# Optimization experiments

Hardware: AMD Instinct MI355X
Metric: run time of the kernel (lower is better)

The kernel has to match this reference:

```python
import jax, jax.numpy as jnp
import numpy as np

N_NODES, N_EDGES, NUM_GRAPHS = 50000, 800000, 64
F_DIM, H_DIM, N_LAYERS, N_CLASSES = 64, 64, 3, 16
EPS = 1e-5  # StdAggregation epsilon (PyG)


def setup_inputs() -> dict:
    key = jax.random.key(0)
    ks = jax.random.split(key, 12)
    s = 0.05
    x = jax.random.normal(ks[0], (N_NODES, F_DIM), jnp.float32)
    edge_index = jax.random.randint(ks[1], (2, N_EDGES), 0, N_NODES, dtype=jnp.int32)
    batch = jnp.sort(jax.random.randint(ks[2], (N_NODES,), 0, NUM_GRAPHS, dtype=jnp.int32))
    # per-layer PNAConv params (towers=1): pre Linear(2F->F), post Linear(13F->H), lin Linear(H->H)
    pre_w = jax.random.normal(ks[3], (N_LAYERS, F_DIM, 2 * F_DIM), jnp.float32) * s
    pre_b = jnp.zeros((N_LAYERS, F_DIM), jnp.float32)
    post_w = jax.random.normal(ks[4], (N_LAYERS, H_DIM, 13 * F_DIM), jnp.float32) * s
    post_b = jnp.zeros((N_LAYERS, H_DIM), jnp.float32)
    lin_w = jax.random.normal(ks[5], (N_LAYERS, H_DIM, H_DIM), jnp.float32) * s
    lin_b = jnp.zeros((N_LAYERS, H_DIM), jnp.float32)
    mlp_w1 = jax.random.normal(ks[6], (H_DIM, H_DIM), jnp.float32) * s
    mlp_b1 = jnp.zeros((H_DIM,), jnp.float32)
    mlp_w2 = jax.random.normal(ks[7], (N_CLASSES, H_DIM), jnp.float32) * s
    mlp_b2 = jnp.zeros((N_CLASSES,), jnp.float32)
    return dict(x=x, edge_index=edge_index, batch=batch,
                pre_w=pre_w, pre_b=pre_b, post_w=post_w, post_b=post_b,
                lin_w=lin_w, lin_b=lin_b, mlp_w1=mlp_w1, mlp_b1=mlp_b1,
                mlp_w2=mlp_w2, mlp_b2=mlp_b2)


def pna_forward(x, src, dst, pre_w, pre_b, post_w, post_b, lin_w, lin_b,
                mlp_w1, mlp_b1, mlp_w2, mlp_b2, batch):
    N = x.shape[0]
    deg_raw = jax.ops.segment_sum(jnp.ones_like(src, jnp.float32), dst, N)  # in-degree [N]
    deg = jnp.maximum(deg_raw, 1.0)[:, None]
    # avg log degree (PNA avg_deg['log'] from the degree histogram of this graph)
    avg_log = jnp.mean(jnp.log(deg_raw + 1.0))
    log_deg = jnp.log(deg + 1.0)
    amp = log_deg / avg_log          # amplification scaler [N,1]
    att = avg_log / log_deg          # attenuation scaler [N,1]
    has_in = (deg_raw > 0)[:, None]

    for l in range(pre_w.shape[0]):
        h = jnp.concatenate([x[dst], x[src]], axis=-1)        # [E, 2F] (x_i, x_j)
        m = h @ pre_w[l].T + pre_b[l]                          # pre_nn message [E, F]
        s1 = jax.ops.segment_sum(m, dst, N)
        s2 = jax.ops.segment_sum(m * m, dst, N)
        mean = s1 / deg
        std = jnp.sqrt(jax.nn.relu(s2 / deg - mean * mean) + EPS)
        mn = jnp.where(has_in, jax.ops.segment_min(m, dst, N), 0.0)
        mx = jnp.where(has_in, jax.ops.segment_max(m, dst, N), 0.0)
        aggr = jnp.concatenate([mean, mn, mx, std], axis=-1)   # [N, 4F]
        out = jnp.concatenate([x, aggr, aggr * amp, aggr * att], axis=-1)  # [N, 13F]
        out = out @ post_w[l].T + post_b[l]                    # post_nn [N, H]
        x = jax.nn.relu(out @ lin_w[l].T + lin_b[l])           # conv.lin + outer ReLU

    # global mean pool over graphs
    counts = jnp.maximum(
        jax.ops.segment_sum(jnp.ones((N,), x.dtype), batch, NUM_GRAPHS), 1.0)
    g = jax.ops.segment_sum(x, batch, NUM_GRAPHS) / counts[:, None]  # [G, H]
    g = jax.nn.relu(g @ mlp_w1.T + mlp_b1)
    return g @ mlp_w2.T + mlp_b2                               # [G, C]


def reference(x, edge_index, batch, pre_w, pre_b, post_w, post_b,
              lin_w, lin_b, mlp_w1, mlp_b1, mlp_w2, mlp_b2):
    src, dst = edge_index[0], edge_index[1]
    return pna_forward(x, src, dst, pre_w, pre_b, post_w, post_b,
                       lin_w, lin_b, mlp_w1, mlp_b1, mlp_w2, mlp_b2, batch)
```

## Files before the change

kernel.cpp:

```cpp
#include <hip/hip_runtime.h>
#include <math.h>

#define N_NODES   50000
#define N_EDGES   800000
#define NUM_GRAPHS 64
#define FDIM      64
#define HDIM      64
#define NLAYERS   3
#define NCLASSES  16
#define EPS       1e-5f

#define SCAN_CHUNK 1024
#define NCHUNKS ((N_NODES + SCAN_CHUNK - 1) / SCAN_CHUNK)

typedef unsigned short u16;
typedef unsigned int   u32;
typedef __attribute__((ext_vector_type(8))) short short8;
typedef __attribute__((ext_vector_type(4))) float floatx4;

#define WKS_LAYER 159744

__device__ inline void split1(float f, u16& h, u16& m, u16& l) {
    u32 b  = __float_as_uint(f);
    u32 hb = b & 0xFFFF0000u;
    float r = f - __uint_as_float(hb);
    u32 mb = __float_as_uint(r) & 0xFFFF0000u;
    float r2 = r - __uint_as_float(mb);
    u32 lb = __float_as_uint(r2) & 0xFFFF0000u;
    h = (u16)(hb >> 16); m = (u16)(mb >> 16); l = (u16)(lb >> 16);
}

__device__ inline void gl_lds16(const void* g, void* l) {
    __builtin_amdgcn_global_load_lds(
        (const __attribute__((address_space(1))) u32*)g,
        (__attribute__((address_space(3))) u32*)l, 16, 0, 0);
}

__global__ __launch_bounds__(256) void k_comb(const float* __restrict__ post_w,
                                              const float* __restrict__ lin_w,
                                              const float* __restrict__ post_b,
                                              const float* __restrict__ lin_b,
                                              u16* __restrict__ WkS,
                                              float* __restrict__ bcv,
                                              int* __restrict__ cnt,
                                              float* __restrict__ logsum) {
    int b = blockIdx.x, t = threadIdx.x;
    int zi = b * 256 + t;
    if (zi < N_NODES) cnt[zi] = 0;
    if (zi == 0) *logsum = 0.f;

    if (b < 624) {
        int c  = t & 63;
        int kl = t >> 6;
        int l  = b / 208;
        int o  = (b % 208) * 4 + kl;
        const float* lw = lin_w + (size_t)l * 4096 + c * 64;
        const float* pw = post_w + (size_t)l * 53248 + o;
        float acc = 0.f;
        #pragma unroll 8
        for (int j = 0; j < 64; ++j)
            acc += lw[j] * pw[(size_t)j * 832];
        u16 h, m, lo;
        split1(acc, h, m, lo);

        int kn;
        if (o < 64) kn = o;
        else {
            int s  = (o - 64) >> 8;
            int mm = (o - 64) & 255;
            int j  = mm >> 5, r = mm & 31;
            kn = 64 + j * 96 + s * 32 + r;
        }
        int ch  = kn >> 5;
        int kin = kn & 31;
        int n16 = c & 15, nt = c >> 4;
        int swk = (((kin >> 3) + (n16 >> 1)) & 3) * 8 + (kin & 7);
        size_t base = (size_t)l * WKS_LAYER + (size_t)ch * 6144
                    + nt * 512 + n16 * 32 + swk;
        WkS[base]        = h;
        WkS[base + 2048] = m;
        WkS[base + 4096] = lo;
    } else if (t < 192) {
        int l = t >> 6, c = t & 63;
        float acc = lin_b[l * 64 + c];
        for (int j = 0; j < 64; ++j)
            acc += lin_w[(size_t)l * 4096 + c * 64 + j] * post_b[l * 64 + j];
        bcv[l * 64 + c] = acc;
    }
}

__global__ void k_count(const int* __restrict__ dst, int* __restrict__ cnt,
                        int* __restrict__ rank) {
    int e = blockIdx.x * 256 + threadIdx.x;
    if (e < N_EDGES) rank[e] = atomicAdd(&cnt[dst[e]], 1);
}

__global__ void k_chunk_sums(const int* __restrict__ cnt, int* __restrict__ bsum,
                             float* __restrict__ logsum) {
    __shared__ int   ired[256];
    __shared__ float lred[256];
    int b = blockIdx.x, t = threadIdx.x;
    int base = b * SCAN_CHUNK;
    int s = 0; float ls = 0.f;
    for (int i = t; i < SCAN_CHUNK; i += 256) {
        int idx = base + i;
        if (idx < N_NODES) {
            int v = cnt[idx];
            s += v;
            ls += logf((float)v + 1.0f);
        }
    }
    ired[t] = s; lred[t] = ls;
    __syncthreads();
    for (int off = 128; off > 0; off >>= 1) {
        if (t < off) { ired[t] += ired[t + off]; lred[t] += lred[t + off]; }
        __syncthreads();
    }
    if (t == 0) { bsum[b] = ired[0]; atomicAdd(logsum, lred[0]); }
}

__global__ void k_scan_top(const int* __restrict__ bsum, int* __restrict__ boff,
                           int* __restrict__ row_start) {
    if (threadIdx.x == 0) {
        int acc = 0;
        for (int i = 0; i < NCHUNKS; ++i) { boff[i] = acc; acc += bsum[i]; }
        row_start[N_NODES] = acc;
    }
}

__global__ void k_scan_chunks(const int* __restrict__ cnt, const int* __restrict__ boff,
                              int* __restrict__ row_start) {
    __shared__ int tsum[256];
    int b = blockIdx.x, t = threadIdx.x;
    int base = b * SCAN_CHUNK + t * 4;
    int v[4]; int s = 0;
    #pragma unroll
    for (int i = 0; i < 4; ++i) {
        int idx = base + i;
        v[i] = (idx < N_NODES) ? cnt[idx] : 0;
        s += v[i];
    }
    tsum[t] = s;
    __syncthreads();
    for (int off = 1; off < 256; off <<= 1) {
        int val = (t >= off) ? tsum[t - off] : 0;
        __syncthreads();
        tsum[t] += val;
        __syncthreads();
    }
    int excl = boff[b] + tsum[t] - s;
    #pragma unroll
    for (int i = 0; i < 4; ++i) {
        int idx = base + i;
        if (idx < N_NODES) row_start[idx] = excl;
        excl += v[i];
    }
}

__global__ void k_scatter(const int* __restrict__ src, const int* __restrict__ dst,
                          const int* __restrict__ rank,
                          const int* __restrict__ row_start,
                          int* __restrict__ csr_src) {
    int e = blockIdx.x * 256 + threadIdx.x;
    if (e < N_EDGES) {
        int d = dst[e];
        csr_src[row_start[d] + rank[e]] = src[e];
    }
}

__global__ void k_scal(const int* __restrict__ cnt, const float* __restrict__ logsum,
                       float* __restrict__ inv_deg, float* __restrict__ ampv,
                       float* __restrict__ attv, float* __restrict__ g_sum,
                       int* __restrict__ g_cnt) {
    int n = blockIdx.x * 256 + threadIdx.x;
    if (blockIdx.x == 0) {
        for (int i = threadIdx.x; i < 4096; i += 256) g_sum[i] = 0.f;
        if (threadIdx.x < 64) g_cnt[threadIdx.x] = 0;
    }
    if (n < N_NODES) {
        float avg = logsum[0] / (float)N_NODES;
        float degf = fmaxf((float)cnt[n], 1.0f);
        inv_deg[n] = 1.0f / degf;
        float ld = logf(degf + 1.0f);
        ampv[n] = ld / avg;
        attv[n] = avg / ld;
    }
}

__global__ __launch_bounds__(256) void k_pre(const float* __restrict__ x,
                                             const float* __restrict__ pre_w,
                                             const float* __restrict__ pre_b,
                                             float* __restrict__ p,
                                             float* __restrict__ q) {
    __shared__ float At[64][68];
    __shared__ float Wt[128][68];
    int t = threadIdx.x;
    int c4 = (t & 15) * 4;
    int r4 = (t >> 4) * 4;
    int rowBase = blockIdx.x * 64;
    int srow = t >> 2, skq = t & 3;

    #pragma unroll
    for (int pass = 0; pass < 4; ++pass) {
        int kk = (pass * 4 + skq) * 4;
        int row = rowBase + srow;
        float4 v = make_float4(0.f, 0.f, 0.f, 0.f);
        if (row < N_NODES) v = *(const float4*)&x[(size_t)row * 64 + kk];
        At[kk + 0][srow] = v.x;
        At[kk + 1][srow] = v.y;
        At[kk + 2][srow] = v.z;
        At[kk + 3][srow] = v.w;
    }
    for (int idx4 = t; idx4 < 2048; idx4 += 256) {
        int c = idx4 & 63, kq = idx4 >> 6;
        float4 v = *(const float4*)&pre_w[(size_t)c * 128 + kq * 4];
        Wt[kq * 4 + 0][c] = v.x;
        Wt[kq * 4 + 1][c] = v.y;
        Wt[kq * 4 + 2][c] = v.z;
        Wt[kq * 4 + 3][c] = v.w;
    }
    __syncthreads();

    float accp[4][4] = {{0}}, accq[4][4] = {{0}};
    #pragma unroll 4
    for (int kk = 0; kk < 64; ++kk) {
        float4 a  = *(const float4*)&At[kk][r4];
        float4 wp = *(const float4*)&Wt[kk][c4];
        float4 wq = *(const float4*)&Wt[64 + kk][c4];
        float av[4]  = {a.x, a.y, a.z, a.w};
        float wpv[4] = {wp.x, wp.y, wp.z, wp.w};
        float wqv[4] = {wq.x, wq.y, wq.z, wq.w};
        #pragma unroll
        for (int i = 0; i < 4; ++i)
            #pragma unroll
            for (int j = 0; j < 4; ++j) {
                accp[i][j] += av[i] * wpv[j];
                accq[i][j] += av[i] * wqv[j];
            }
    }
    float pb[4];
    #pragma unroll
    for (int j = 0; j < 4; ++j) pb[j] = pre_b[c4 + j];
    #pragma unroll
    for (int i = 0; i < 4; ++i) {
        int row = rowBase + r4 + i;
        if (row < N_NODES) {
            float4 vp = make_float4(accp[i][0] + pb[0], accp[i][1] + pb[1],
                                    accp[i][2] + pb[2], accp[i][3] + pb[3]);
            float4 vq = make_float4(accq[i][0], accq[i][1], accq[i][2], accq[i][3]);
            *(float4*)&p[row * 64 + c4] = vp;
            *(float4*)&q[row * 64 + c4] = vq;
        }
    }
}

__global__ __launch_bounds__(256) void k_aggr(const float* __restrict__ p,
                                              const float* __restrict__ q,
                                              const int* __restrict__ row_start,
                                              const int* __restrict__ csr_src,
                                              const float* __restrict__ inv_deg,
                                              float* __restrict__ aggr) {
    int wid  = (blockIdx.x * 256 + threadIdx.x) >> 6;
    int lane = threadIdx.x & 63;
    if (wid >= N_NODES) return;
    int n = wid;
    int beg = row_start[n], end = row_start[n + 1];
    float sum = 0.f, sq = 0.f;
    float mn = INFINITY, mx = -INFINITY;
    int e = beg;
    for (; e + 7 < end; e += 8) {
        float qv[8];
        #pragma unroll
        for (int u = 0; u < 8; ++u) {
            int s = csr_src[e + u];
            qv[u] = q[(size_t)s * 64 + lane];
        }
        #pragma unroll
        for (int u = 0; u < 8; ++u) {
            float m = qv[u];
            sum += m; sq += m * m;
            mn = fminf(mn, m); mx = fmaxf(mx, m);
        }
    }
    for (; e + 3 < end; e += 4) {
        float qv[4];
        #pragma unroll
        for (int u = 0; u < 4; ++u) {
            int s = csr_src[e + u];
            qv[u] = q[(size_t)s * 64 + lane];
        }
        #pragma unroll
        for (int u = 0; u < 4; ++u) {
            float m = qv[u];
            sum += m; sq += m * m;
            mn = fminf(mn, m); mx = fmaxf(mx, m);
        }
    }
    for (; e < end; ++e) {
        int s = csr_src[e];
        float m = q[(size_t)s * 64 + lane];
        sum += m; sq += m * m;
        mn = fminf(mn, m); mx = fmaxf(mx, m);
    }
    float* a = aggr + (size_t)n * 256;
    if (end <= beg) {
        a[lane]       = 0.f;
        a[64 + lane]  = 0.f;
        a[128 + lane] = 0.f;
        a[192 + lane] = sqrtf(EPS);
    } else {
        float pv = p[n * 64 + lane];
        float id = inv_deg[n];
        float meanq = sum * id;
        float var = fmaxf(sq * id - meanq * meanq, 0.f);
        a[lane]       = pv + meanq;
        a[64 + lane]  = pv + mn;
        a[128 + lane] = pv + mx;
        a[192 + lane] = sqrtf(var + EPS);
    }
}

__global__ __launch_bounds__(256, 4) void k_post(const float* __restrict__ x,
                                                 const float* __restrict__ aggr,
                                                 const float* __restrict__ ampv,
                                                 const float* __restrict__ attv,
                                                 const u16* __restrict__ WkS,
                                                 const float* __restrict__ bc,
                                                 float* __restrict__ xout) {
    __shared__ u16 ldsB[3 * 6144];
    int t = threadIdx.x;
    int w = t >> 6;
    int lane = t & 63;
    int m = lane & 15;
    int qh = lane >> 4;
    int rowBase = blockIdx.x * 64;

    int myrow = rowBase + 16 * w + m;
    bool vr = myrow < N_NODES;
    int crow = vr ? myrow : 0;
    float ampR = vr ? ampv[crow] : 0.f;
    float attR = vr ? attv[crow] : 0.f;
    const float* xrow = x + (size_t)crow * 64;
    const float* arow = aggr + (size_t)crow * 256;

    int bo = m * 32 + ((qh + (m >> 1)) & 3) * 8;

    floatx4 acc[4] = {};
    float fc[8], fn[8];

    auto aptr = [&](int ch) -> const float* {
        if (ch <= 0) return xrow;
        if (ch == 1) return xrow + 32;
        int j = (ch - 2) / 3;
        if (j > 7) j = 7;
        return arow + j * 32;
    };
    auto loadRaw = [&](const float* sp, float* f) {
        float4 u0 = *(const float4*)(sp + qh * 8);
        float4 u1 = *(const float4*)(sp + qh * 8 + 4);
        f[0] = vr ? u0.x : 0.f; f[1] = vr ? u0.y : 0.f;
        f[2] = vr ? u0.z : 0.f; f[3] = vr ? u0.w : 0.f;
        f[4] = vr ? u1.x : 0.f; f[5] = vr ? u1.y : 0.f;
        f[6] = vr ? u1.z : 0.f; f[7] = vr ? u1.w : 0.f;
    };
    auto stageIssue = [&](int ch, int buf) {
        const char* g = (const char*)WkS + (size_t)ch * 12288 + w * 3072 + lane * 16;
        char* l = (char*)ldsB + buf * 12288 + w * 3072;
        #pragma unroll
        for (int i = 0; i < 3; ++i)
            gl_lds16(g + i * 1024, l + i * 1024);
    };

    loadRaw(aptr(0), fc);
    stageIssue(0, 0);
    stageIssue(1, 1);
    asm volatile("s_waitcnt vmcnt(3)" ::: "memory");
    asm volatile("s_barrier" ::: "memory");

    for (int ch = 0; ch < 26; ++ch) {
        loadRaw(aptr(ch + 1), fn);
        int ch2 = (ch + 2 < 26) ? ch + 2 : ch + 2 - 26;
        stageIssue(ch2, (ch + 2) % 3);

        float sc = 1.f;
        if (ch >= 2) {
            int s = (ch - 2) % 3;
            sc = (s == 0) ? 1.f : ((s == 1) ? ampR : attR);
        }

        union { u32 u[4]; short8 s8; } AH, AM, AL;
        #pragma unroll
        for (int i = 0; i < 4; ++i) {
            float f0 = fc[2 * i] * sc, f1 = fc[2 * i + 1] * sc;
            u32 b0 = __float_as_uint(f0), b1 = __float_as_uint(f1);
            u32 h0 = b0 & 0xFFFF0000u,  h1 = b1 & 0xFFFF0000u;
            float r0 = f0 - __uint_as_float(h0);
            float r1 = f1 - __uint_as_float(h1);
            u32 m0 = __float_as_uint(r0) & 0xFFFF0000u;
            u32 m1 = __float_as_uint(r1) & 0xFFFF0000u;
            float s0 = r0 - __uint_as_float(m0);
            float s1 = r1 - __uint_as_float(m1);
            u32 l0 = __float_as_uint(s0) & 0xFFFF0000u;
            u32 l1 = __float_as_uint(s1) & 0xFFFF0000u;
            AH.u[i] = (h0 >> 16) | h1;
            AM.u[i] = (m0 >> 16) | m1;
            AL.u[i] = (l0 >> 16) | l1;
        }

        const u16* Bb = ldsB + (ch % 3) * 6144;
        #pragma unroll
        for (int nt = 0; nt < 4; ++nt) {
            short8 bH = *(const short8*)(Bb + nt * 512 + bo);
            short8 bM = *(const short8*)(Bb + 2048 + nt * 512 + bo);
            short8 bL = *(const short8*)(Bb + 4096 + nt * 512 + bo);
            acc[nt] = __builtin_amdgcn_mfma_f32_16x16x32_bf16(AH.s8, bH, acc[nt], 0, 0, 0);
            acc[nt] = __builtin_amdgcn_mfma_f32_16x16x32_bf16(AH.s8, bM, acc[nt], 0, 0, 0);
            acc[nt] = __builtin_amdgcn_mfma_f32_16x16x32_bf16(AM.s8, bH, acc[nt], 0, 0, 0);
            acc[nt] = __builtin_amdgcn_mfma_f32_16x16x32_bf16(AH.s8, bL, acc[nt], 0, 0, 0);
            acc[nt] = __builtin_amdgcn_mfma_f32_16x16x32_bf16(AM.s8, bM, acc[nt], 0, 0, 0);
            acc[nt] = __builtin_amdgcn_mfma_f32_16x16x32_bf16(AL.s8, bH, acc[nt], 0, 0, 0);
        }

        asm volatile("s_waitcnt vmcnt(5)" ::: "memory");
        asm volatile("s_barrier" ::: "memory");

        #pragma unroll
        for (int i = 0; i < 8; ++i) fc[i] = fn[i];
    }

    int col = lane & 15;
    #pragma unroll
    for (int nt = 0; nt < 4; ++nt) {
        float bias = bc[nt * 16 + col];
        #pragma unroll
        for (int reg = 0; reg < 4; ++reg) {
            int grow = rowBase + 16 * w + qh * 4 + reg;
            if (grow < N_NODES) {
                xout[(size_t)grow * 64 + nt * 16 + col] =
                    fmaxf(acc[nt][reg] + bias, 0.f);
            }
        }
    }
}

__global__ __launch_bounds__(256) void k_pool(const float* __restrict__ x,
                                              const int* __restrict__ batch,
                                              float* __restrict__ g_sum,
                                              int* __restrict__ g_cnt) {
    int lane = threadIdx.x & 63;
    int wave = blockIdx.x * 4 + (threadIdx.x >> 6);
    const int NPW = 16;
    int beg = wave * NPW;
    if (beg >= N_NODES) return;
    int end = min(beg + NPW, N_NODES);
    float acc = 0.f;
    int cur = batch[beg];
    int c = 0;
    for (int n = beg; n < end; ++n) {
        int b = batch[n];
        if (b != cur) {
            atomicAdd(&g_sum[cur * 64 + lane], acc);
            if (lane == 0) atomicAdd(&g_cnt[cur], c);
            acc = 0.f; c = 0; cur = b;
        }
        acc += x[n * 64 + lane];
        ++c;
    }
    atomicAdd(&g_sum[cur * 64 + lane], acc);
    if (lane == 0) atomicAdd(&g_cnt[cur], c);
}

__global__ __launch_bounds__(256) void k_mlp(const float* __restrict__ g_sum,
                                             const int* __restrict__ g_cnt,
                                             const float* __restrict__ w1,
                                             const float* __restrict__ b1,
                                             const float* __restrict__ w2,
                                             const float* __restrict__ b2,
                                             float* __restrict__ out) {
    __shared__ float g[64][64];
    __shared__ float h[64][64];
    __shared__ float wT[64][65];
    int t = threadIdx.x;
    for (int idx = t; idx < 4096; idx += 256) {
        int gi = idx >> 6, c = idx & 63;
        float cntf = fmaxf((float)g_cnt[gi], 1.f);
        g[gi][c] = g_sum[idx] / cntf;
    }
    for (int idx = t; idx < 4096; idx += 256) {
        int c = idx >> 6, k = idx & 63;
        wT[k][c] = w1[c * 64 + k];
    }
    __syncthreads();
    for (int idx = t; idx < 4096; idx += 256) {
        int gi = idx >> 6, c = idx & 63;
        float acc = b1[c];
        for (int k = 0; k < 64; ++k) acc += g[gi][k] * wT[k][c];
        h[gi][c] = fmaxf(acc, 0.f);
    }
    __syncthreads();
    for (int idx = t; idx < 64 * NCLASSES; idx += 256) {
        int gi = idx >> 4, c = idx & 15;
        float acc = b2[c];
        for (int k = 0; k < 64; ++k) acc += h[gi][k] * w2[c * 64 + k];
        out[gi * NCLASSES + c] = acc;
    }
}

extern "C" void kernel_launch(void* const* d_in, const int* in_sizes, int n_in,
                              void* d_out, int out_size, void* d_ws, size_t ws_size,
                              hipStream_t stream) {
    const float* x      = (const float*)d_in[0];
    const int*   ei     = (const int*)d_in[1];
    const int*   batch  = (const int*)d_in[2];
    const float* pre_w  = (const float*)d_in[3];
    const float* pre_b  = (const float*)d_in[4];
    const float* post_w = (const float*)d_in[5];
    const float* post_b = (const float*)d_in[6];
    const float* lin_w  = (const float*)d_in[7];
    const float* lin_b  = (const float*)d_in[8];
    const float* mlp_w1 = (const float*)d_in[9];
    const float* mlp_b1 = (const float*)d_in[10];
    const float* mlp_w2 = (const float*)d_in[11];
    const float* mlp_b2 = (const float*)d_in[12];

    const int* src = ei;
    const int* dst = ei + N_EDGES;

    char* base = (char*)d_ws;
    size_t off = 0;
    auto alloc = [&](size_t bytes) -> void* {
        void* ptr = base + off;
        off += (bytes + 255) & ~(size_t)255;
        return ptr;
    };
    int*   cnt       = (int*)alloc(N_NODES * 4);
    int*   row_start = (int*)alloc((N_NODES + 1) * 4);
    int*   rank      = (int*)alloc(N_EDGES * 4);
    int*   csr_src   = (int*)alloc(N_EDGES * 4);
    int*   bsum      = (int*)alloc(64 * 4);
    int*   boff      = (int*)alloc(64 * 4);
    float* logsum    = (float*)alloc(16);
    float* inv_deg   = (float*)alloc(N_NODES * 4);
    float* ampv      = (float*)alloc(N_NODES * 4);
    float* attv      = (float*)alloc(N_NODES * 4);
    float* p         = (float*)alloc((size_t)N_NODES * 64 * 4);
    float* q         = (float*)alloc((size_t)N_NODES * 64 * 4);
    float* aggr      = (float*)alloc((size_t)N_NODES * 256 * 4);
    float* xb0       = (float*)alloc((size_t)N_NODES * 64 * 4);
    float* xb1       = (float*)alloc((size_t)N_NODES * 64 * 4);
    float* g_sum     = (float*)alloc(64 * 64 * 4);
    int*   g_cnt     = (int*)alloc(64 * 4);
    u16*   WkS       = (u16*)alloc((size_t)3 * WKS_LAYER * 2);
    float* bcv       = (float*)alloc(3 * 64 * 4);

    k_comb<<<625, 256, 0, stream>>>(post_w, lin_w, post_b, lin_b, WkS, bcv,
                                    cnt, logsum);

    k_count<<<(N_EDGES + 255) / 256, 256, 0, stream>>>(dst, cnt, rank);
    k_chunk_sums<<<NCHUNKS, 256, 0, stream>>>(cnt, bsum, logsum);
    k_scan_top<<<1, 64, 0, stream>>>(bsum, boff, row_start);
    k_scan_chunks<<<NCHUNKS, 256, 0, stream>>>(cnt, boff, row_start);
    k_scatter<<<(N_EDGES + 255) / 256, 256, 0, stream>>>(src, dst, rank,
                                                         row_start, csr_src);
    k_scal<<<(N_NODES + 255) / 256, 256, 0, stream>>>(cnt, logsum, inv_deg,
                                                      ampv, attv, g_sum, g_cnt);

    const int GEMM_BLOCKS = (N_NODES + 63) / 64;
    const float* xin = x;
    float* bufs[3] = {xb0, xb1, xb0};
    for (int l = 0; l < NLAYERS; ++l) {
        k_pre<<<GEMM_BLOCKS, 256, 0, stream>>>(xin, pre_w + (size_t)l * 64 * 128,
                                               pre_b + l * 64, p, q);
        k_aggr<<<(N_NODES + 3) / 4, 256, 0, stream>>>(p, q, row_start, csr_src,
                                                      inv_deg, aggr);
        float* xo = bufs[l];
        k_post<<<GEMM_BLOCKS, 256, 0, stream>>>(xin, aggr, ampv, attv,
                                                WkS + (size_t)l * WKS_LAYER,
                                                bcv + l * 64, xo);
        xin = xo;
    }

    int pool_waves = (N_NODES + 15) / 16;
    k_pool<<<(pool_waves + 3) / 4, 256, 0, stream>>>(xin, batch, g_sum, g_cnt);
    k_mlp<<<1, 256, 0, stream>>>(g_sum, g_cnt, mlp_w1, mlp_b1, mlp_w2, mlp_b2,
                                 (float*)d_out);
}
```

Baseline: 491.5 us.

## Move pre-linear GEMM to split-bf16 MFMA with pre-swizzled weights

Replaces the FP32 SIMT register-tiled k_pre GEMM with a bf16x3 split MFMA version that keeps near-fp32 accuracy, using six MFMA products per tile. The pre_w weights are split into hi/mid/lo bf16 parts and swizzled once in k_comb, which gets extra blocks for this. In k_pre they are loaded straight to LDS with global_load_lds. The goal is to lower compute time in the per-layer pre GEMM. The cost is extra split arithmetic, and the output stores become scalar strided writes instead of float4.

```diff
diff --git a/kernel.cpp b/kernel.cpp
--- a/kernel.cpp
+++ b/kernel.cpp
@@ -19,6 +19,7 @@
 typedef __attribute__((ext_vector_type(4))) float floatx4;
 
 #define WKS_LAYER 159744
+#define PRES_LAYER 24576
 
 __device__ inline void split1(float f, u16& h, u16& m, u16& l) {
     u32 b  = __float_as_uint(f);
@@ -38,9 +39,11 @@
 
 __global__ __launch_bounds__(256) void k_comb(const float* __restrict__ post_w,
                                               const float* __restrict__ lin_w,
+                                              const float* __restrict__ pre_w,
                                               const float* __restrict__ post_b,
                                               const float* __restrict__ lin_b,
                                               u16* __restrict__ WkS,
+                                              u16* __restrict__ PreS,
                                               float* __restrict__ bcv,
                                               int* __restrict__ cnt,
                                               float* __restrict__ logsum) {
@@ -80,12 +83,33 @@
         WkS[base]        = h;
         WkS[base + 2048] = m;
         WkS[base + 4096] = lo;
-    } else if (t < 192) {
-        int l = t >> 6, c = t & 63;
-        float acc = lin_b[l * 64 + c];
-        for (int j = 0; j < 64; ++j)
-            acc += lin_w[(size_t)l * 4096 + c * 64 + j] * post_b[l * 64 + j];
-        bcv[l * 64 + c] = acc;
+    } else if (b == 624) {
+        if (t < 192) {
+            int l = t >> 6, c = t & 63;
+            float acc = lin_b[l * 64 + c];
+            for (int j = 0; j < 64; ++j)
+                acc += lin_w[(size_t)l * 4096 + c * 64 + j] * post_b[l * 64 + j];
+            bcv[l * 64 + c] = acc;
+        }
+    } else {
+        int i = (b - 625) * 256 + t;
+        int l = i >> 13;
+        int rem = i & 8191;
+        int c128 = rem >> 6;
+        int k = rem & 63;
+        float v;
+        if (c128 < 64) v = pre_w[(size_t)l * 8192 + c128 * 128 + k];
+        else           v = pre_w[(size_t)l * 8192 + (c128 - 64) * 128 + 64 + k];
+        u16 h, m, lo;
+        split1(v, h, m, lo);
+        int ch = k >> 5, kin = k & 31;
+        int nt = c128 >> 4, n16 = c128 & 15;
+        int swk = (((kin >> 3) + (n16 >> 1)) & 3) * 8 + (kin & 7);
+        size_t base = (size_t)l * PRES_LAYER + (size_t)ch * 12288
+                    + nt * 512 + n16 * 32 + swk;
+        PreS[base]        = h;
+        PreS[base + 4096] = m;
+        PreS[base + 8192] = lo;
     }
 }
 
@@ -187,69 +211,95 @@
     }
 }
 
-__global__ __launch_bounds__(256) void k_pre(const float* __restrict__ x,
-                                             const float* __restrict__ pre_w,
-                                             const float* __restrict__ pre_b,
-                                             float* __restrict__ p,
-                                             float* __restrict__ q) {
-    __shared__ float At[64][68];
-    __shared__ float Wt[128][68];
+__global__ __launch_bounds__(256, 4) void k_pre(const float* __restrict__ x,
+                                                const u16* __restrict__ PreS,
+                                                const float* __restrict__ pre_b,
+                                                float* __restrict__ p,
+                                                float* __restrict__ q) {
+    __shared__ u16 ldsB[2 * 12288];
     int t = threadIdx.x;
-    int c4 = (t & 15) * 4;
-    int r4 = (t >> 4) * 4;
+    int w = t >> 6;
+    int lane = t & 63;
+    int m = lane & 15;
+    int qh = lane >> 4;
     int rowBase = blockIdx.x * 64;
-    int srow = t >> 2, skq = t & 3;
+
+    int myrow = rowBase + 16 * w + m;
+    bool vr = myrow < N_NODES;
+    int crow = vr ? myrow : 0;
+    const float* xrow = x + (size_t)crow * 64;
+
+    int bo = m * 32 + ((qh + (m >> 1)) & 3) * 8;
 
     #pragma unroll
-    for (int pass = 0; pass < 4; ++pass) {
-        int kk = (pass * 4 + skq) * 4;
-        int row = rowBase + srow;
-        float4 v = make_float4(0.f, 0.f, 0.f, 0.f);
-        if (row < N_NODES) v = *(const float4*)&x[(size_t)row * 64 + kk];
-        At[kk + 0][srow] = v.x;
-        At[kk + 1][srow] = v.y;
-        At[kk + 2][srow] = v.z;
-        At[kk + 3][srow] = v.w;
-    }
-    for (int idx4 = t; idx4 < 2048; idx4 += 256) {
-        int c = idx4 & 63, kq = idx4 >> 6;
-        float4 v = *(const float4*)&pre_w[(size_t)c * 128 + kq * 4];
-        Wt[kq * 4 + 0][c] = v.x;
-        Wt[kq * 4 + 1][c] = v.y;
-        Wt[kq * 4 + 2][c] = v.z;
-        Wt[kq * 4 + 3][c] = v.w;
-    }
+    for (int ch = 0; ch < 2; ++ch) {
+        const char* g = (const char*)PreS + (size_t)ch * 24576 + w * 6144 + lane * 16;
+        char* l = (char*)ldsB + ch * 24576 + w * 6144;
+        #pragma unroll
+        for (int i = 0; i < 6; ++i)
+            gl_lds16(g + i * 1024, l + i * 1024);
+    }
+    float fa[2][8];
+    #pragma unroll
+    for (int ch = 0; ch < 2; ++ch) {
+        const float* sp = xrow + ch * 32 + qh * 8;
+        float4 u0 = *(const float4*)sp;
+        float4 u1 = *(const float4*)(sp + 4);
+        fa[ch][0] = vr ? u0.x : 0.f; fa[ch][1] = vr ? u0.y : 0.f;
+        fa[ch][2] = vr ? u0.z : 0.f; fa[ch][3] = vr ? u0.w : 0.f;
+        fa[ch][4] = vr ? u1.x : 0.f; fa[ch][5] = vr ? u1.y : 0.f;
+        fa[ch][6] = vr ? u1.z : 0.f; fa[ch][7] = vr ? u1.w : 0.f;
+    }
+    asm volatile("s_waitcnt vmcnt(0)" ::: "memory");
     __syncthreads();
 
-    float accp[4][4] = {{0}}, accq[4][4] = {{0}};
-    #pragma unroll 4
-    for (int kk = 0; kk < 64; ++kk) {
-        float4 a  = *(const float4*)&At[kk][r4];
-        float4 wp = *(const float4*)&Wt[kk][c4];
-        float4 wq = *(const float4*)&Wt[64 + kk][c4];
-        float av[4]  = {a.x, a.y, a.z, a.w};
-        float wpv[4] = {wp.x, wp.y, wp.z, wp.w};
-        float wqv[4] = {wq.x, wq.y, wq.z, wq.w};
-        #pragma unroll
-        for (int i = 0; i < 4; ++i)
-            #pragma unroll
-            for (int j = 0; j < 4; ++j) {
-                accp[i][j] += av[i] * wpv[j];
-                accq[i][j] += av[i] * wqv[j];
-            }
-    }
-    float pb[4];
+    floatx4 acc[8] = {};
     #pragma unroll
-    for (int j = 0; j < 4; ++j) pb[j] = pre_b[c4 + j];
+    for (int ch = 0; ch < 2; ++ch) {
+        union { u32 u[4]; short8 s8; } AH, AM, AL;
+        #pragma unroll
+        for (int i = 0; i < 4; ++i) {
+            float f0 = fa[ch][2 * i], f1 = fa[ch][2 * i + 1];
+            u32 b0 = __float_as_uint(f0), b1 = __float_as_uint(f1);
+            u32 h0 = b0 & 0xFFFF0000u,  h1 = b1 & 0xFFFF0000u;
+            float r0 = f0 - __uint_as_float(h0);
+            float r1 = f1 - __uint_as_float(h1);
+            u32 m0 = __float_as_uint(r0) & 0xFFFF0000u;
+            u32 m1 = __float_as_uint(r1) & 0xFFFF0000u;
+            float s0 = r0 - __uint_as_float(m0);
+            float s1 = r1 - __uint_as_float(m1);
+            u32 l0 = __float_as_uint(s0) & 0xFFFF0000u;
+            u32 l1 = __float_as_uint(s1) & 0xFFFF0000u;
+            AH.u[i] = (h0 >> 16) | h1;
+            AM.u[i] = (m0 >> 16) | m1;
+            AL.u[i] = (l0 >> 16) | l1;
+        }
+        const u16* Bb = ldsB + ch * 12288;
+        #pragma unroll
+        for (int nt = 0; nt < 8; ++nt) {
+            short8 bH = *(const short8*)(Bb + nt * 512 + bo);
+            short8 bM = *(const short8*)(Bb + 4096 + nt * 512 + bo);
+            short8 bL = *(const short8*)(Bb + 8192 + nt * 512 + bo);
+            acc[nt] = __builtin_amdgcn_mfma_f32_16x16x32_bf16(AH.s8, bH, acc[nt], 0, 0, 0);
+            acc[nt] = __builtin_amdgcn_mfma_f32_16x16x32_bf16(AH.s8, bM, acc[nt], 0, 0, 0);
+            acc[nt] = __builtin_amdgcn_mfma_f32_16x16x32_bf16(AM.s8, bH, acc[nt], 0, 0, 0);
+            acc[nt] = __builtin_amdgcn_mfma_f32_16x16x32_bf16(AH.s8, bL, acc[nt], 0, 0, 0);
+            acc[nt] = __builtin_amdgcn_mfma_f32_16x16x32_bf16(AM.s8, bM, acc[nt], 0, 0, 0);
+            acc[nt] = __builtin_amdgcn_mfma_f32_16x16x32_bf16(AL.s8, bH, acc[nt], 0, 0, 0);
+        }
+    }
+
+    int col = m;
     #pragma unroll
-    for (int i = 0; i < 4; ++i) {
-        int row = rowBase + r4 + i;
-        if (row < N_NODES) {
-            float4 vp = make_float4(accp[i][0] + pb[0], accp[i][1] + pb[1],
-                                    accp[i][2] + pb[2], accp[i][3] + pb[3]);
-            float4 vq = make_float4(accq[i][0], accq[i][1], accq[i][2], accq[i][3]);
-            *(float4*)&p[row * 64 + c4] = vp;
-            *(float4*)&q[row * 64 + c4] = vq;
+    for (int nt = 0; nt < 8; ++nt) {
+        int cbase = (nt & 3) * 16 + col;
+        float bias = (nt < 4) ? pre_b[cbase] : 0.f;
+        float* outp = (nt < 4) ? p : q;
+        #pragma unroll
+        for (int reg = 0; reg < 4; ++reg) {
+            int grow = rowBase + 16 * w + qh * 4 + reg;
+            if (grow < N_NODES)
+                outp[(size_t)grow * 64 + cbase] = acc[nt][reg] + bias;
         }
     }
 }
@@ -551,10 +601,11 @@
     float* g_sum     = (float*)alloc(64 * 64 * 4);
     int*   g_cnt     = (int*)alloc(64 * 4);
     u16*   WkS       = (u16*)alloc((size_t)3 * WKS_LAYER * 2);
+    u16*   PreS      = (u16*)alloc((size_t)3 * PRES_LAYER * 2);
     float* bcv       = (float*)alloc(3 * 64 * 4);
 
-    k_comb<<<625, 256, 0, stream>>>(post_w, lin_w, post_b, lin_b, WkS, bcv,
-                                    cnt, logsum);
+    k_comb<<<721, 256, 0, stream>>>(post_w, lin_w, pre_w, post_b, lin_b,
+                                    WkS, PreS, bcv, cnt, logsum);
 
     k_count<<<(N_EDGES + 255) / 256, 256, 0, stream>>>(dst, cnt, rank);
     k_chunk_sums<<<NCHUNKS, 256, 0, stream>>>(cnt, bsum, logsum);
@@ -569,7 +620,7 @@
     const float* xin = x;
     float* bufs[3] = {xb0, xb1, xb0};
     for (int l = 0; l < NLAYERS; ++l) {
-        k_pre<<<GEMM_BLOCKS, 256, 0, stream>>>(xin, pre_w + (size_t)l * 64 * 128,
+        k_pre<<<GEMM_BLOCKS, 256, 0, stream>>>(xin, PreS + (size_t)l * PRES_LAYER,
                                                pre_b + l * 64, p, q);
         k_aggr<<<(N_NODES + 3) / 4, 256, 0, stream>>>(p, q, row_start, csr_src,
                                                       inv_deg, aggr);
```

Result: faster. 469.8 us (-4.4%).
